# Kernel optimization log

Measured on AMD Instinct MI355X. Metric: run time of the kernel, lower is better.

Reference implementation:

```python
import jax, jax.numpy as jnp
import numpy as np

N_FUNS = 10  # subset of SYMBOLIC_LIB safe on all of R

def _apply_funs(z, fun_ids):
    # z: (batch, out, in); fun_ids: (out, in) int ids selecting the symbolic fn
    branches = [
        z,                      # 0: 'x'
        z * z,                  # 1: 'x^2'
        z * z * z,              # 2: 'x^3'
        jnp.sin(z),             # 3: 'sin'
        jnp.tanh(z),            # 4: 'tanh'
        jax.nn.sigmoid(z),      # 5: 'sigmoid'
        jnp.exp(-z * z),        # 6: 'gaussian'
        jnp.abs(z),             # 7: 'abs'
        jnp.arctan(z),          # 8: 'arctan'
        jnp.exp(z),             # 9: 'exp'
    ]
    ids = fun_ids[None, :, :]  # broadcast over batch
    return jnp.select([ids == k for k in range(N_FUNS)], branches)


def setup_inputs() -> dict:
    key = jax.random.key(0)
    k1, k2, k3 = jax.random.split(key, 3)
    batch, in_f, out_f = 4096, 128, 128
    x = jax.random.normal(k1, (batch, in_f), dtype=jnp.float32)
    affine = jax.random.normal(k2, (out_f, in_f, 4), dtype=jnp.float32)
    mask = jnp.eye(in_f, dtype=jnp.float32)  # default buffer: identity
    fun_ids = jax.random.randint(k3, (out_f, in_f), 0, N_FUNS, dtype=jnp.int32)
    return {"x": x, "affine": affine, "mask": mask, "fun_ids": fun_ids}


def reference(x, affine, mask, fun_ids):
    # reduce inputs through the mask (identity by default): (batch, reduced_in)
    x_red = jnp.einsum("bi,ri->br", x, mask)
    a = affine[None, :, :, 0]  # (1, out, in)
    b = affine[None, :, :, 1]
    c = affine[None, :, :, 2]
    d = affine[None, :, :, 3]
    z = a * x_red[:, None, :] + b          # (batch, out, in)
    postacts = c * _apply_funs(z, fun_ids) + d  # (batch, out, in)
    y = jnp.sum(postacts, axis=2)           # (batch, out)
    return y, postacts
```

## Files before the change

kernel.cpp:

```cpp
#include <hip/hip_runtime.h>
#include <cmath>

#define BATCH_DIV 64
#define XR_BB     16

__global__ __launch_bounds__(256) void xred_kernel(const float* __restrict__ x,
                                                   const float* __restrict__ mask,
                                                   float* __restrict__ xred) {
    __shared__ float ms[128][129];
    __shared__ float xs[128][20];
    const int tid   = threadIdx.x;
    const int bbase = blockIdx.x * XR_BB;

    const float4* m4 = (const float4*)mask;
    for (int k = tid; k < 4096; k += 256) {
        float4 v = m4[k];
        int row = k >> 5;
        int col = (k & 31) * 4;
        ms[row][col]     = v.x;
        ms[row][col + 1] = v.y;
        ms[row][col + 2] = v.z;
        ms[row][col + 3] = v.w;
    }
    for (int k = tid; k < XR_BB * 128; k += 256) {
        int b = k >> 7, i = k & 127;
        xs[i][b] = x[(size_t)(bbase + b) * 128 + i];
    }
    __syncthreads();

    const int r = tid & 127;
    const int g = tid >> 7;
    float acc[8] = {0.f, 0.f, 0.f, 0.f, 0.f, 0.f, 0.f, 0.f};
    for (int i = 0; i < 128; ++i) {
        const float  m  = ms[r][i];
        const float4 xa = *(const float4*)&xs[i][8 * g];
        const float4 xb = *(const float4*)&xs[i][8 * g + 4];
        acc[0] += m * xa.x; acc[1] += m * xa.y; acc[2] += m * xa.z; acc[3] += m * xa.w;
        acc[4] += m * xb.x; acc[5] += m * xb.y; acc[6] += m * xb.z; acc[7] += m * xb.w;
    }
    #pragma unroll
    for (int j = 0; j < 8; ++j)
        xred[(size_t)(bbase + 8 * g + j) * 128 + r] = acc[j];
}

__global__ __launch_bounds__(256) void kan_main(const float2* __restrict__ xred,
                                                const float4* __restrict__ affine,
                                                const int* __restrict__ fun_ids,
                                                float* __restrict__ y,
                                                float2* __restrict__ postacts) {
    const int tid  = threadIdx.x;
    const int lane = tid & 63;
    const int w    = tid >> 6;
    const int o    = blockIdx.x;
    const int i0   = 2 * lane;
    const int i1   = 2 * lane + 1;

    const float4 A0 = affine[o * 128 + i0];
    const float4 A1 = affine[o * 128 + i1];
    const int    f0 = fun_ids[o * 128 + i0];
    const int    f1 = fun_ids[o * 128 + i1];

    const bool m1_0 = (f0 == 1), m2_0 = (f0 == 2), m7_0 = (f0 == 7), m3_0 = (f0 == 3), m8_0 = (f0 == 8);
    const bool m1_1 = (f1 == 1), m2_1 = (f1 == 2), m7_1 = (f1 == 7), m3_1 = (f1 == 3), m8_1 = (f1 == 8);
    const bool me_0 = (f0 >= 4 && f0 <= 6) || (f0 == 9);
    const bool me_1 = (f1 >= 4 && f1 <= 6) || (f1 == 9);

    float k1_0 = 0.f, k2_0 = 0.f, An_0 = 0.f, Bn_0 = 1.f, Dd_0 = 0.f;
    if      (f0 == 4) { k1_0 = -2.f; An_0 = 1.f; Bn_0 = -1.f; Dd_0 = 1.f; }
    else if (f0 == 5) { k1_0 = -1.f; An_0 = 1.f; Bn_0 =  0.f; Dd_0 = 1.f; }
    else if (f0 == 6) { k2_0 = -1.f; }
    else if (f0 == 9) { k1_0 =  1.f; }
    float k1_1 = 0.f, k2_1 = 0.f, An_1 = 0.f, Bn_1 = 1.f, Dd_1 = 0.f;
    if      (f1 == 4) { k1_1 = -2.f; An_1 = 1.f; Bn_1 = -1.f; Dd_1 = 1.f; }
    else if (f1 == 5) { k1_1 = -1.f; An_1 = 1.f; Bn_1 =  0.f; Dd_1 = 1.f; }
    else if (f1 == 6) { k2_1 = -1.f; }
    else if (f1 == 9) { k1_1 =  1.f; }

    const int bbase = blockIdx.y * BATCH_DIV + w;

    for (int it = 0; it < BATCH_DIV / 4; ++it) {
        const int b = bbase + 4 * it;
        const float2 xr = xred[(size_t)b * 64 + lane];

        float p0;
        {
            const float z  = fmaf(A0.x, xr.x, A0.y);
            const float zz = z * z;
            float p = m1_0 ? zz : z;
            p = m2_0 ? zz * z : p;
            p = m7_0 ? fabsf(z) : p;
            const float s = __sinf(z);
            p = m3_0 ? s : p;
            float arg = fminf(fmaf(k2_0, zz, k1_0 * z), 80.f);
            const float e   = __expf(arg);
            const float num = fmaf(Bn_0, e, An_0);
            const float den = fmaf(Dd_0, e, 1.0f);
            const float r   = num * __builtin_amdgcn_rcpf(den);
            p = me_0 ? r : p;
            const float az  = fabsf(z);
            const bool  big = az > 1.0f;
            const float t   = big ? __builtin_amdgcn_rcpf(az) : az;
            const float t2  = t * t;
            float q = fmaf(t2, -0.01172120f, 0.05265332f);
            q = fmaf(t2, q, -0.11643287f);
            q = fmaf(t2, q,  0.19354346f);
            q = fmaf(t2, q, -0.33262347f);
            q = fmaf(t2, q,  0.99997726f);
            q = t * q;
            q = big ? 1.57079632679f - q : q;
            const float at = copysignf(q, z);
            p = m8_0 ? at : p;
            p0 = fmaf(A0.z, p, A0.w);
        }
        float p1;
        {
            const float z  = fmaf(A1.x, xr.y, A1.y);
            const float zz = z * z;
            float p = m1_1 ? zz : z;
            p = m2_1 ? zz * z : p;
            p = m7_1 ? fabsf(z) : p;
            const float s = __sinf(z);
            p = m3_1 ? s : p;
            float arg = fminf(fmaf(k2_1, zz, k1_1 * z), 80.f);
            const float e   = __expf(arg);
            const float num = fmaf(Bn_1, e, An_1);
            const float den = fmaf(Dd_1, e, 1.0f);
            const float r   = num * __builtin_amdgcn_rcpf(den);
            p = me_1 ? r : p;
            const float az  = fabsf(z);
            const bool  big = az > 1.0f;
            const float t   = big ? __builtin_amdgcn_rcpf(az) : az;
            const float t2  = t * t;
            float q = fmaf(t2, -0.01172120f, 0.05265332f);
            q = fmaf(t2, q, -0.11643287f);
            q = fmaf(t2, q,  0.19354346f);
            q = fmaf(t2, q, -0.33262347f);
            q = fmaf(t2, q,  0.99997726f);
            q = t * q;
            q = big ? 1.57079632679f - q : q;
            const float at = copysignf(q, z);
            p = m8_1 ? at : p;
            p1 = fmaf(A1.z, p, A1.w);
        }

        postacts[((size_t)b * 128 + o) * 64 + lane] = make_float2(p0, p1);

        float s = p0 + p1;
        #pragma unroll
        for (int off = 32; off > 0; off >>= 1) s += __shfl_down(s, off, 64);
        if (lane == 0) y[(size_t)b * 128 + o] = s;
    }
}

extern "C" void kernel_launch(void* const* d_in, const int* in_sizes, int n_in,
                              void* d_out, int out_size, void* d_ws, size_t ws_size,
                              hipStream_t stream) {
    const float* x       = (const float*)d_in[0];
    const float* affine  = (const float*)d_in[1];
    const float* mask    = (const float*)d_in[2];
    const int*   fun_ids = (const int*)d_in[3];

    const int batch = in_sizes[0] / 128;

    float* xred     = (float*)d_ws;
    float* y        = (float*)d_out;
    float* postacts = y + (size_t)batch * 128;

    xred_kernel<<<dim3(batch / XR_BB), dim3(256), 0, stream>>>(x, mask, xred);

    kan_main<<<dim3(128, batch / BATCH_DIV), dim3(256), 0, stream>>>(
        (const float2*)xred, (const float4*)affine, fun_ids, y, (float2*)postacts);
}
```

Baseline: 304.5 us.

## Remap kan_main threads to 4 inputs each across 8 outputs per block

Result: no change. 301.4 us (-1.0%).

```diff
diff --git a/kernel.cpp b/kernel.cpp
--- a/kernel.cpp
+++ b/kernel.cpp
@@ -1,8 +1,9 @@
 #include <hip/hip_runtime.h>
 #include <cmath>
 
-#define BATCH_DIV 64
-#define XR_BB     16
+#define XR_BB   16
+#define OGROUP  8
+#define BCHUNK  16
 
 __global__ __launch_bounds__(256) void xred_kernel(const float* __restrict__ x,
                                                    const float* __restrict__ mask,
@@ -43,60 +44,62 @@
         xred[(size_t)(bbase + 8 * g + j) * 128 + r] = acc[j];
 }
 
-__global__ __launch_bounds__(256) void kan_main(const float2* __restrict__ xred,
-                                                const float4* __restrict__ affine,
-                                                const int* __restrict__ fun_ids,
-                                                float* __restrict__ y,
-                                                float2* __restrict__ postacts) {
-    const int tid  = threadIdx.x;
-    const int lane = tid & 63;
-    const int w    = tid >> 6;
-    const int o    = blockIdx.x;
-    const int i0   = 2 * lane;
-    const int i1   = 2 * lane + 1;
+__global__ __launch_bounds__(256, 4) void kan_main(const float4* __restrict__ xred4,
+                                                   const float4* __restrict__ affine,
+                                                   const int* __restrict__ fun_ids,
+                                                   float* __restrict__ y,
+                                                   float4* __restrict__ post4) {
+    const int tid = threadIdx.x;
+    const int oo  = tid >> 5;
+    const int il  = tid & 31;
+    const int o   = blockIdx.x * OGROUP + oo;
 
-    const float4 A0 = affine[o * 128 + i0];
-    const float4 A1 = affine[o * 128 + i1];
-    const int    f0 = fun_ids[o * 128 + i0];
-    const int    f1 = fun_ids[o * 128 + i1];
+    float4 A[4]; int f[4];
+    #pragma unroll
+    for (int j = 0; j < 4; ++j) {
+        A[j] = affine[(size_t)o * 128 + il * 4 + j];
+        f[j] = fun_ids[(size_t)o * 128 + il * 4 + j];
+    }
 
-    const bool m1_0 = (f0 == 1), m2_0 = (f0 == 2), m7_0 = (f0 == 7), m3_0 = (f0 == 3), m8_0 = (f0 == 8);
-    const bool m1_1 = (f1 == 1), m2_1 = (f1 == 2), m7_1 = (f1 == 7), m3_1 = (f1 == 3), m8_1 = (f1 == 8);
-    const bool me_0 = (f0 >= 4 && f0 <= 6) || (f0 == 9);
-    const bool me_1 = (f1 >= 4 && f1 <= 6) || (f1 == 9);
+    bool m1[4], m2[4], m3[4], m7[4], m8[4], me[4];
+    float k1[4], k2[4], An[4], Bn[4], Dd[4];
+    #pragma unroll
+    for (int j = 0; j < 4; ++j) {
+        const int fj = f[j];
+        m1[j] = (fj == 1); m2[j] = (fj == 2); m3[j] = (fj == 3);
+        m7[j] = (fj == 7); m8[j] = (fj == 8);
+        me[j] = (fj >= 4 && fj <= 6) || (fj == 9);
+        float k1v = 0.f, k2v = 0.f, Anv = 0.f, Bnv = 1.f, Ddv = 0.f;
+        if      (fj == 4) { k1v = -2.f; Anv = 1.f; Bnv = -1.f; Ddv = 1.f; }
+        else if (fj == 5) { k1v = -1.f; Anv = 1.f; Bnv =  0.f; Ddv = 1.f; }
+        else if (fj == 6) { k2v = -1.f; }
+        else if (fj == 9) { k1v =  1.f; }
+        k1[j] = k1v; k2[j] = k2v; An[j] = Anv; Bn[j] = Bnv; Dd[j] = Ddv;
+    }
 
-    float k1_0 = 0.f, k2_0 = 0.f, An_0 = 0.f, Bn_0 = 1.f, Dd_0 = 0.f;
-    if      (f0 == 4) { k1_0 = -2.f; An_0 = 1.f; Bn_0 = -1.f; Dd_0 = 1.f; }
-    else if (f0 == 5) { k1_0 = -1.f; An_0 = 1.f; Bn_0 =  0.f; Dd_0 = 1.f; }
-    else if (f0 == 6) { k2_0 = -1.f; }
-    else if (f0 == 9) { k1_0 =  1.f; }
-    float k1_1 = 0.f, k2_1 = 0.f, An_1 = 0.f, Bn_1 = 1.f, Dd_1 = 0.f;
-    if      (f1 == 4) { k1_1 = -2.f; An_1 = 1.f; Bn_1 = -1.f; Dd_1 = 1.f; }
-    else if (f1 == 5) { k1_1 = -1.f; An_1 = 1.f; Bn_1 =  0.f; Dd_1 = 1.f; }
-    else if (f1 == 6) { k2_1 = -1.f; }
-    else if (f1 == 9) { k1_1 =  1.f; }
+    const int b0 = blockIdx.y * BCHUNK;
 
-    const int bbase = blockIdx.y * BATCH_DIV + w;
+    for (int bb = 0; bb < BCHUNK; ++bb) {
+        const int b = b0 + bb;
+        const float4 xr = xred4[(size_t)b * 32 + il];
+        const float xv[4] = {xr.x, xr.y, xr.z, xr.w};
 
-    for (int it = 0; it < BATCH_DIV / 4; ++it) {
-        const int b = bbase + 4 * it;
-        const float2 xr = xred[(size_t)b * 64 + lane];
-
-        float p0;
-        {
-            const float z  = fmaf(A0.x, xr.x, A0.y);
+        float p[4];
+        #pragma unroll
+        for (int j = 0; j < 4; ++j) {
+            const float z  = fmaf(A[j].x, xv[j], A[j].y);
             const float zz = z * z;
-            float p = m1_0 ? zz : z;
-            p = m2_0 ? zz * z : p;
-            p = m7_0 ? fabsf(z) : p;
+            float pv = m1[j] ? zz : z;
+            pv = m2[j] ? zz * z : pv;
+            pv = m7[j] ? fabsf(z) : pv;
             const float s = __sinf(z);
-            p = m3_0 ? s : p;
-            float arg = fminf(fmaf(k2_0, zz, k1_0 * z), 80.f);
+            pv = m3[j] ? s : pv;
+            const float arg = fminf(fmaf(k2[j], zz, k1[j] * z), 80.f);
             const float e   = __expf(arg);
-            const float num = fmaf(Bn_0, e, An_0);
-            const float den = fmaf(Dd_0, e, 1.0f);
+            const float num = fmaf(Bn[j], e, An[j]);
+            const float den = fmaf(Dd[j], e, 1.0f);
             const float r   = num * __builtin_amdgcn_rcpf(den);
-            p = me_0 ? r : p;
+            pv = me[j] ? r : pv;
             const float az  = fabsf(z);
             const bool  big = az > 1.0f;
             const float t   = big ? __builtin_amdgcn_rcpf(az) : az;
@@ -109,46 +112,19 @@
             q = t * q;
             q = big ? 1.57079632679f - q : q;
             const float at = copysignf(q, z);
-            p = m8_0 ? at : p;
-            p0 = fmaf(A0.z, p, A0.w);
-        }
-        float p1;
-        {
-            const float z  = fmaf(A1.x, xr.y, A1.y);
-            const float zz = z * z;
-            float p = m1_1 ? zz : z;
-            p = m2_1 ? zz * z : p;
-            p = m7_1 ? fabsf(z) : p;
-            const float s = __sinf(z);
-            p = m3_1 ? s : p;
-            float arg = fminf(fmaf(k2_1, zz, k1_1 * z), 80.f);
-            const float e   = __expf(arg);
-            const float num = fmaf(Bn_1, e, An_1);
-            const float den = fmaf(Dd_1, e, 1.0f);
-            const float r   = num * __builtin_amdgcn_rcpf(den);
-            p = me_1 ? r : p;
-            const float az  = fabsf(z);
-            const bool  big = az > 1.0f;
-            const float t   = big ? __builtin_amdgcn_rcpf(az) : az;
-            const float t2  = t * t;
-            float q = fmaf(t2, -0.01172120f, 0.05265332f);
-            q = fmaf(t2, q, -0.11643287f);
-            q = fmaf(t2, q,  0.19354346f);
-            q = fmaf(t2, q, -0.33262347f);
-            q = fmaf(t2, q,  0.99997726f);
-            q = t * q;
-            q = big ? 1.57079632679f - q : q;
-            const float at = copysignf(q, z);
-            p = m8_1 ? at : p;
-            p1 = fmaf(A1.z, p, A1.w);
+            pv = m8[j] ? at : pv;
+            p[j] = fmaf(A[j].z, pv, A[j].w);
         }
 
-        postacts[((size_t)b * 128 + o) * 64 + lane] = make_float2(p0, p1);
+        post4[((size_t)b * 128 + o) * 32 + il] = make_float4(p[0], p[1], p[2], p[3]);
 
-        float s = p0 + p1;
-        #pragma unroll
-        for (int off = 32; off > 0; off >>= 1) s += __shfl_down(s, off, 64);
-        if (lane == 0) y[(size_t)b * 128 + o] = s;
+        float s = (p[0] + p[1]) + (p[2] + p[3]);
+        s += __shfl_xor(s, 1, 64);
+        s += __shfl_xor(s, 2, 64);
+        s += __shfl_xor(s, 4, 64);
+        s += __shfl_xor(s, 8, 64);
+        s += __shfl_xor(s, 16, 64);
+        if (il == 0) y[(size_t)b * 128 + o] = s;
     }
 }
 
@@ -168,6 +144,6 @@
 
     xred_kernel<<<dim3(batch / XR_BB), dim3(256), 0, stream>>>(x, mask, xred);
 
-    kan_main<<<dim3(128, batch / BATCH_DIV), dim3(256), 0, stream>>>(
-        (const float2*)xred, (const float4*)affine, fun_ids, y, (float2*)postacts);
+    kan_main<<<dim3(128 / OGROUP, batch / BCHUNK), dim3(256), 0, stream>>>(
+        (const float4*)xred, (const float4*)affine, fun_ids, y, (float4*)postacts);
 }
```
